# Kernel tuning notes

Hardware: AMD Instinct MI355X
Metric: run time of the kernel (lower is better)

Reference implementation:

```python
import jax, jax.numpy as jnp
import numpy as np

N_NODES = 50000
N_EDGES = 800000
IN_CH = 64
HID = 64
EDGE_DIM = 16


def _glorot(key, shape):
    fan_in, fan_out = shape[0], shape[1]
    lim = (6.0 / (fan_in + fan_out)) ** 0.5
    return jax.random.uniform(key, shape, jnp.float32, -lim, lim)


def setup_inputs() -> dict:
    key = jax.random.key(0)
    ks = jax.random.split(key, 12)
    x = jax.random.normal(ks[0], (N_NODES, IN_CH), jnp.float32)
    edge_index = jax.random.randint(ks[1], (2, N_EDGES), 0, N_NODES, jnp.int64)
    edge_attr = jax.random.normal(ks[2], (N_EDGES, EDGE_DIM), jnp.float32)
    # SAGEConv1: lin_l (aggregated neighbors, with bias) + lin_r (root, no bias)
    W1l = _glorot(ks[3], (IN_CH, HID)); b1l = jnp.zeros((HID,), jnp.float32)
    W1r = _glorot(ks[4], (IN_CH, HID))
    # SAGEConv2
    W2l = _glorot(ks[5], (HID, HID)); b2l = jnp.zeros((HID,), jnp.float32)
    W2r = _glorot(ks[6], (HID, HID))
    # edge MLP: Linear(2*HID+EDGE_DIM -> HID), ReLU, Linear(HID -> 1)
    Wm1 = _glorot(ks[7], (2 * HID + EDGE_DIM, HID))
    bm1 = jnp.zeros((HID,), jnp.float32)
    Wm2 = _glorot(ks[8], (HID, 1))
    bm2 = jnp.zeros((1,), jnp.float32)
    return dict(x=x, edge_index=edge_index, edge_attr=edge_attr,
                W1l=W1l, b1l=b1l, W1r=W1r,
                W2l=W2l, b2l=b2l, W2r=W2r,
                Wm1=Wm1, bm1=bm1, Wm2=Wm2, bm2=bm2)


def _sage_conv(x, src, dst, deg_inv, Wl, bl, Wr):
    # mean aggregation of source-node features at destination nodes
    n = x.shape[0]
    agg = jax.ops.segment_sum(x[src], dst, num_segments=n)  # [N, d]
    agg = agg * deg_inv  # mean over incoming edges
    return agg @ Wl + bl + x @ Wr


def reference(x, edge_index, edge_attr, W1l, b1l, W1r, W2l, b2l, W2r, Wm1, bm1, Wm2, bm2):
    src, dst = edge_index[0], edge_index[1]
    n = x.shape[0]
    # in-degree (over dst), clamped to 1 as in PyG mean aggregation
    deg = jax.ops.segment_sum(jnp.ones((src.shape[0],), x.dtype), dst, num_segments=n)
    deg_inv = (1.0 / jnp.maximum(deg, 1.0))[:, None]  # [N,1]

    h = jax.nn.relu(_sage_conv(x, src, dst, deg_inv, W1l, b1l, W1r))
    h = jax.nn.relu(_sage_conv(h, src, dst, deg_inv, W2l, b2l, W2r))

    # gather endpoint embeddings + concat with edge features -> MLP score
    edge_input = jnp.concatenate([h[src], h[dst], edge_attr], axis=-1)  # [E, 2H+De]
    hidden = jax.nn.relu(edge_input @ Wm1 + bm1)
    return (hidden @ Wm2 + bm2).squeeze(-1)  # [E]
```

## Files before the change

### kernel.cpp

```cpp
#include <hip/hip_runtime.h>
#include <hip/hip_bf16.h>


#define C 64
#define KP 168
#define SK 136
#define TILE_E 64
#define WSHIFT 12

typedef short short8 __attribute__((ext_vector_type(8)));
typedef float f32x4 __attribute__((ext_vector_type(4)));

__device__ __forceinline__ unsigned short f2bf(float f) {
    unsigned int u = __float_as_uint(f);
    return (unsigned short)((u + 0x7FFFu + ((u >> 16) & 1u)) >> 16);
}
__device__ __forceinline__ unsigned int pack2(float lo, float hi) {
    return (unsigned int)f2bf(lo) | ((unsigned int)f2bf(hi) << 16);
}
__device__ __forceinline__ float bflo(unsigned int u) { return __uint_as_float(u << 16); }
__device__ __forceinline__ float bfhi(unsigned int u) { return __uint_as_float(u & 0xFFFF0000u); }

__global__ void prep(const int* __restrict__ dst, int* __restrict__ degi,
                     const float* __restrict__ ea, unsigned short* __restrict__ eaB,
                     const float* __restrict__ x, unsigned short* __restrict__ xB,
                     int E, int nx8, int doEa) {
    int i = blockIdx.x * blockDim.x + threadIdx.x;
    if (i < E) atomicAdd(&degi[dst[i]], 1);
    if (doEa && i < 2 * E) {
        const float4* p = (const float4*)(ea + (size_t)i * 8);
        float4 a = p[0], b = p[1];
        uint4 o;
        o.x = pack2(a.x, a.y); o.y = pack2(a.z, a.w);
        o.z = pack2(b.x, b.y); o.w = pack2(b.z, b.w);
        *(uint4*)(eaB + (size_t)i * 8) = o;
    }
    if (i < nx8) {
        const float4* p = (const float4*)(x + (size_t)i * 8);
        float4 a = p[0], b = p[1];
        uint4 o;
        o.x = pack2(a.x, a.y); o.y = pack2(a.z, a.w);
        o.z = pack2(b.x, b.y); o.w = pack2(b.z, b.w);
        *(uint4*)(xB + (size_t)i * 8) = o;
    }
}

__global__ __launch_bounds__(256) void scan_partial(const int* __restrict__ degi,
        int* __restrict__ rowptr, int* __restrict__ partials, int N) {
    __shared__ int sWs[4];
    int t = threadIdx.x, b = blockIdx.x;
    int g0 = b * 1024 + t * 4;
    int v0 = (g0 + 0 < N) ? degi[g0 + 0] : 0;
    int v1 = (g0 + 1 < N) ? degi[g0 + 1] : 0;
    int v2 = (g0 + 2 < N) ? degi[g0 + 2] : 0;
    int v3 = (g0 + 3 < N) ? degi[g0 + 3] : 0;
    int tsum = v0 + v1 + v2 + v3;
    int lane = t & 63, w = t >> 6;
    int incl = tsum;
    #pragma unroll
    for (int m = 1; m < 64; m <<= 1) {
        int y = __shfl_up(incl, m, 64);
        if (lane >= m) incl += y;
    }
    if (lane == 63) sWs[w] = incl;
    __syncthreads();
    int wprefix = 0;
    for (int i = 0; i < w; ++i) wprefix += sWs[i];
    int run = wprefix + incl - tsum;
    if (g0 + 0 < N) rowptr[g0 + 0] = run; run += v0;
    if (g0 + 1 < N) rowptr[g0 + 1] = run; run += v1;
    if (g0 + 2 < N) rowptr[g0 + 2] = run; run += v2;
    if (g0 + 3 < N) rowptr[g0 + 3] = run;
    if (t == 255) partials[b] = wprefix + incl;
}

__global__ __launch_bounds__(256) void scan_add_fused(int* __restrict__ rowptr,
        const int* __restrict__ partials, int* __restrict__ cursor,
        const int* __restrict__ degi, float* __restrict__ deg_inv,
        int N, int E, int nb) {
    __shared__ int sOff[64];
    int t = threadIdx.x;
    if (t < 64) {
        int v = (t < nb) ? partials[t] : 0;
        int incl = v;
        #pragma unroll
        for (int m = 1; m < 64; m <<= 1) {
            int y = __shfl_up(incl, m, 64);
            if (t >= m) incl += y;
        }
        sOff[t] = incl - v;
    }
    __syncthreads();
    int i = blockIdx.x * 256 + t;
    if (i < N) {
        int r = rowptr[i] + sOff[i >> 10];
        rowptr[i] = r;
        cursor[i] = r;
        deg_inv[i] = 1.0f / fmaxf((float)degi[i], 1.0f);
    }
    if (i == 0) rowptr[N] = E;
}

__global__ __launch_bounds__(256) void fill_csr_xcd(const int* __restrict__ src,
        const int* __restrict__ dst, int* __restrict__ cursor,
        int* __restrict__ eSrc, int E) {
    int g = blockIdx.x & 7;
    int tid = (blockIdx.x >> 3) * 256 + threadIdx.x;
    int stride = (gridDim.x >> 3) * 256;
    for (int e = tid; e < E; e += stride) {
        int d = dst[e];
        if (((d >> WSHIFT) & 7) == g) {
            int pos = atomicAdd(&cursor[d], 1);
            eSrc[pos] = src[e];
        }
    }
}

__global__ __launch_bounds__(256) void csr_agg_np(const unsigned short* __restrict__ fB,
        const int* __restrict__ rowptr, const int* __restrict__ eSrc,
        const float* __restrict__ deg_inv, unsigned short* __restrict__ aggB, int N) {
    int wv = threadIdx.x >> 6;
    int lane = threadIdx.x & 63;
    int nl = lane & 7, cg = lane >> 3;
    int node = blockIdx.x * 32 + wv * 8 + nl;
    if (node >= N) return;
    int row = rowptr[node], end = rowptr[node + 1];
    float a[8] = {0.f, 0.f, 0.f, 0.f, 0.f, 0.f, 0.f, 0.f};
    int j = row;
    for (; j + 2 <= end; j += 2) {
        int s0 = eSrc[j];
        int s1 = eSrc[j + 1];
        uint4 v0 = *(const uint4*)(fB + (size_t)s0 * C + cg * 8);
        uint4 v1 = *(const uint4*)(fB + (size_t)s1 * C + cg * 8);
        a[0] += bflo(v0.x); a[1] += bfhi(v0.x);
        a[2] += bflo(v0.y); a[3] += bfhi(v0.y);
        a[4] += bflo(v0.z); a[5] += bfhi(v0.z);
        a[6] += bflo(v0.w); a[7] += bfhi(v0.w);
        a[0] += bflo(v1.x); a[1] += bfhi(v1.x);
        a[2] += bflo(v1.y); a[3] += bfhi(v1.y);
        a[4] += bflo(v1.z); a[5] += bfhi(v1.z);
        a[6] += bflo(v1.w); a[7] += bfhi(v1.w);
    }
    if (j < end) {
        int s = eSrc[j];
        uint4 v = *(const uint4*)(fB + (size_t)s * C + cg * 8);
        a[0] += bflo(v.x); a[1] += bfhi(v.x);
        a[2] += bflo(v.y); a[3] += bfhi(v.y);
        a[4] += bflo(v.z); a[5] += bfhi(v.z);
        a[6] += bflo(v.w); a[7] += bfhi(v.w);
    }
    float di = deg_inv[node];
    uint4 o;
    o.x = pack2(a[0] * di, a[1] * di);
    o.y = pack2(a[2] * di, a[3] * di);
    o.z = pack2(a[4] * di, a[5] * di);
    o.w = pack2(a[6] * di, a[7] * di);
    *(uint4*)(aggB + (size_t)node * C + cg * 8) = o;
}

__global__ __launch_bounds__(256) void dense_mfma(
        const unsigned short* __restrict__ aB, const unsigned short* __restrict__ xB,
        const float* __restrict__ Wl, const float* __restrict__ Wr,
        const float* __restrict__ bl, unsigned short* __restrict__ hOut, int N) {
    __shared__ unsigned short sW[C * SK];
    __shared__ unsigned short sAB[C * SK];
    int t = threadIdx.x;
    int lane = t & 63, w = t >> 6;
    int l15 = lane & 15, quad = lane >> 4;
    int n0 = blockIdx.x * 64;

    for (int i = t; i < 128 * C; i += 256) {
        int k = i >> 6, n = i & 63;
        float v = (k < C) ? Wl[k * C + n] : Wr[(k - C) * C + n];
        sW[n * SK + k] = f2bf(v);
    }
    for (int i = t; i < 64 * 16; i += 256) {
        int r = i >> 4, ch = i & 15;
        int node = n0 + r;
        uint4 v = {0u, 0u, 0u, 0u};
        if (node < N)
            v = (ch < 8) ? *(const uint4*)(aB + (size_t)node * C + ch * 8)
                         : *(const uint4*)(xB + (size_t)node * C + (ch - 8) * 8);
        *(uint4*)&sAB[r * SK + ch * 8] = v;
    }
    __syncthreads();

    short8 bW[4][4];
    #pragma unroll
    for (int t4 = 0; t4 < 4; ++t4)
        #pragma unroll
        for (int kc = 0; kc < 4; ++kc)
            bW[t4][kc] = *(const short8*)&sW[(t4 * 16 + l15) * SK + kc * 32 + quad * 8];
    float blr[4];
    #pragma unroll
    for (int t4 = 0; t4 < 4; ++t4) blr[t4] = bl[t4 * 16 + l15];

    f32x4 acc[4] = {{0.f, 0.f, 0.f, 0.f}, {0.f, 0.f, 0.f, 0.f},
                    {0.f, 0.f, 0.f, 0.f}, {0.f, 0.f, 0.f, 0.f}};
    #pragma unroll
    for (int kc = 0; kc < 4; ++kc) {
        short8 a = *(const short8*)&sAB[(w * 16 + l15) * SK + kc * 32 + quad * 8];
        #pragma unroll
        for (int t4 = 0; t4 < 4; ++t4)
            acc[t4] = __builtin_amdgcn_mfma_f32_16x16x32_bf16(a, bW[t4][kc], acc[t4], 0, 0, 0);
    }
    __syncthreads();

    #pragma unroll
    for (int t4 = 0; t4 < 4; ++t4)
        #pragma unroll
        for (int r = 0; r < 4; ++r) {
            int rl = w * 16 + quad * 4 + r;
            sW[rl * 72 + t4 * 16 + l15] = f2bf(fmaxf(acc[t4][r] + blr[t4], 0.f));
        }
    __syncthreads();
    for (int i = t; i < 64 * 8; i += 256) {
        int r = i >> 3, c8 = i & 7;
        int node = n0 + r;
        if (node < N)
            *(uint4*)(hOut + (size_t)node * C + c8 * 8) = *(const uint4*)&sW[r * 72 + c8 * 8];
    }
}

template <bool EAB>
__device__ __forceinline__ void gather_rows(const unsigned short* __restrict__ hB,
        const unsigned short* __restrict__ eaB, const float* __restrict__ ea,
        int s, int d, int idxc, int quad,
        uint4& u0, uint4& u1, uint4& u2, uint4& u3, uint4& u4) {
    const uint4* ps = (const uint4*)(hB + (size_t)s * C);
    const uint4* pd = (const uint4*)(hB + (size_t)d * C);
    u0 = ps[quad];
    u1 = ps[4 + quad];
    u2 = pd[quad];
    u3 = pd[4 + quad];
    u4.x = 0u; u4.y = 0u; u4.z = 0u; u4.w = 0u;
    if (quad < 2) {
        if (EAB) {
            u4 = *(const uint4*)(eaB + (size_t)idxc * 16 + quad * 8);
        } else {
            const float4* pe = (const float4*)(ea + (size_t)idxc * 16 + quad * 8);
            float4 f0 = pe[0], f1 = pe[1];
            u4.x = pack2(f0.x, f0.y); u4.y = pack2(f0.z, f0.w);
            u4.z = pack2(f1.x, f1.y); u4.w = pack2(f1.z, f1.w);
        }
    }
}

template <bool EAB>
__global__ __launch_bounds__(256) void edge_mlp_pipe(
        const unsigned short* __restrict__ hB, const int* __restrict__ src,
        const int* __restrict__ dst, const float* __restrict__ ea,
        const unsigned short* __restrict__ eaB,
        const float* __restrict__ Wm1, const float* __restrict__ bm1,
        const float* __restrict__ Wm2, const float* __restrict__ bm2,
        float* __restrict__ out, int E, int nTiles) {
    __shared__ unsigned short sW[C * KP];
    int t = threadIdx.x;
    int lane = t & 63, w = t >> 6;
    int l15 = lane & 15, quad = lane >> 4;

    for (int i = t; i < C * 3; i += 256) {
        int r = i / 3, cc = 144 + (i % 3) * 8;
        uint4 z = {0u, 0u, 0u, 0u};
        *(uint4*)&sW[r * KP + cc] = z;
    }
    for (int i = t; i < 144 * C; i += 256) {
        int k = i >> 6, n = i & 63;
        sW[n * KP + k] = f2bf(Wm1[i]);
    }
    __syncthreads();

    short8 bW[4][5];
    #pragma unroll
    for (int t4 = 0; t4 < 4; ++t4)
        #pragma unroll
        for (int kc = 0; kc < 5; ++kc)
            bW[t4][kc] = *(const short8*)&sW[(t4 * 16 + l15) * KP + kc * 32 + quad * 8];
    float bmr[4], w2r[4];
    #pragma unroll
    for (int t4 = 0; t4 < 4; ++t4) {
        int j = t4 * 16 + l15;
        bmr[t4] = bm1[j];
        w2r[t4] = Wm2[j];
    }
    float bb = bm2[0];

    int stride = gridDim.x;
    int lbase = w * 16 + l15;

    int tile = blockIdx.x;
    int idxc = min(tile * TILE_E + lbase, E - 1);
    int s = src[idxc], d = dst[idxc];
    int tileN = tile + stride;
    int idxNc = (tileN < nTiles) ? min(tileN * TILE_E + lbase, E - 1) : idxc;
    int sN = src[idxNc], dN = dst[idxNc];
    uint4 cu0, cu1, cu2, cu3, cu4;
    gather_rows<EAB>(hB, eaB, ea, s, d, idxc, quad, cu0, cu1, cu2, cu3, cu4);

    while (true) {
        bool hasNext = (tileN < nTiles);
        uint4 nu0, nu1, nu2, nu3, nu4;
        gather_rows<EAB>(hB, eaB, ea, sN, dN, idxNc, quad, nu0, nu1, nu2, nu3, nu4);
        int tileNN = tileN + stride;
        int idxNNc = (tileNN < nTiles) ? min(tileNN * TILE_E + lbase, E - 1) : idxNc;
        int sNN = src[idxNNc], dNN = dst[idxNNc];

        short8 a0 = *(short8*)&cu0, a1 = *(short8*)&cu1, a2 = *(short8*)&cu2,
               a3 = *(short8*)&cu3, a4 = *(short8*)&cu4;
        f32x4 acc[4] = {{0.f, 0.f, 0.f, 0.f}, {0.f, 0.f, 0.f, 0.f},
                        {0.f, 0.f, 0.f, 0.f}, {0.f, 0.f, 0.f, 0.f}};
        #pragma unroll
        for (int t4 = 0; t4 < 4; ++t4) {
            acc[t4] = __builtin_amdgcn_mfma_f32_16x16x32_bf16(a0, bW[t4][0], acc[t4], 0, 0, 0);
            acc[t4] = __builtin_amdgcn_mfma_f32_16x16x32_bf16(a1, bW[t4][1], acc[t4], 0, 0, 0);
            acc[t4] = __builtin_amdgcn_mfma_f32_16x16x32_bf16(a2, bW[t4][2], acc[t4], 0, 0, 0);
            acc[t4] = __builtin_amdgcn_mfma_f32_16x16x32_bf16(a3, bW[t4][3], acc[t4], 0, 0, 0);
            acc[t4] = __builtin_amdgcn_mfma_f32_16x16x32_bf16(a4, bW[t4][4], acc[t4], 0, 0, 0);
        }

        float sres[4];
        #pragma unroll
        for (int r = 0; r < 4; ++r) {
            float v = 0.f;
            #pragma unroll
            for (int t4 = 0; t4 < 4; ++t4)
                v += fmaxf(acc[t4][r] + bmr[t4], 0.f) * w2r[t4];
            #pragma unroll
            for (int m = 1; m < 16; m <<= 1)
                v += __shfl_xor(v, m, 16);
            sres[r] = v;
        }
        if (l15 == 0) {
            int e0 = tile * TILE_E;
            #pragma unroll
            for (int r = 0; r < 4; ++r) {
                int e = e0 + w * 16 + quad * 4 + r;
                if (e < E) out[e] = sres[r] + bb;
            }
        }

        if (!hasNext) break;
        tile = tileN; tileN = tileNN;
        idxc = idxNc; idxNc = idxNNc;
        s = sN; sN = sNN; d = dN; dN = dNN;
        cu0 = nu0; cu1 = nu1; cu2 = nu2; cu3 = nu3; cu4 = nu4;
    }
}

extern "C" void kernel_launch(void* const* d_in, const int* in_sizes, int n_in,
                              void* d_out, int out_size, void* d_ws, size_t ws_size,
                              hipStream_t stream) {
    const float* x   = (const float*)d_in[0];
    const int*   ei  = (const int*)d_in[1];
    const float* ea  = (const float*)d_in[2];
    const float* W1l = (const float*)d_in[3];
    const float* b1l = (const float*)d_in[4];
    const float* W1r = (const float*)d_in[5];
    const float* W2l = (const float*)d_in[6];
    const float* b2l = (const float*)d_in[7];
    const float* W2r = (const float*)d_in[8];
    const float* Wm1 = (const float*)d_in[9];
    const float* bm1 = (const float*)d_in[10];
    const float* Wm2 = (const float*)d_in[11];
    const float* bm2 = (const float*)d_in[12];
    float* out = (float*)d_out;

    const int N = in_sizes[0] / C;
    const int E = in_sizes[1] / 2;
    const int* src = ei;
    const int* dst = ei + E;

    char* wsb = (char*)d_ws;
    int npad = (N + 1023) & ~1023;
    float* deg_inv = (float*)wsb;                wsb += (size_t)npad * 4;
    unsigned short* xB   = (unsigned short*)wsb; wsb += (size_t)npad * C * 2;
    unsigned short* h1B  = (unsigned short*)wsb; wsb += (size_t)npad * C * 2;
    unsigned short* h2B  = (unsigned short*)wsb; wsb += (size_t)npad * C * 2;
    unsigned short* aggB = (unsigned short*)wsb; wsb += (size_t)npad * C * 2;
    int* degi    = (int*)wsb;                    wsb += (size_t)npad * 4;
    int* rowptr  = (int*)wsb;                    wsb += (size_t)(npad + 64) * 4;
    int* cursor  = (int*)wsb;                    wsb += (size_t)npad * 4;
    int* eSrc    = (int*)wsb;                    wsb += (size_t)E * 4;
    int* partials = (int*)wsb;                   wsb += 64 * 4;
    unsigned short* eaB = (unsigned short*)wsb;
    size_t used = (size_t)(wsb - (char*)d_ws);
    int useEaB = (ws_size >= used + (size_t)E * 16 * 2) ? 1 : 0;

    int tpb = 256;
    int nb = (N + 1023) / 1024;
    int nx8 = N * C / 8;

    hipMemsetAsync(degi, 0, (size_t)N * sizeof(int), stream);
    int prepN = (2 * E > nx8) ? 2 * E : nx8;
    prep<<<(prepN + tpb - 1) / tpb, tpb, 0, stream>>>(dst, degi, ea, eaB, x, xB, E, nx8, useEaB);
    scan_partial<<<nb, tpb, 0, stream>>>(degi, rowptr, partials, N);
    scan_add_fused<<<(N + tpb - 1) / tpb, tpb, 0, stream>>>(rowptr, partials, cursor,
            degi, deg_inv, N, E, nb);
    fill_csr_xcd<<<2048, tpb, 0, stream>>>(src, dst, cursor, eSrc, E);

    int aggGrid = (N + 31) / 32;
    csr_agg_np<<<aggGrid, tpb, 0, stream>>>(xB, rowptr, eSrc, deg_inv, aggB, N);
    dense_mfma<<<(N + 63) / 64, tpb, 0, stream>>>(aggB, xB, W1l, W1r, b1l, h1B, N);

    csr_agg_np<<<aggGrid, tpb, 0, stream>>>(h1B, rowptr, eSrc, deg_inv, aggB, N);
    dense_mfma<<<(N + 63) / 64, tpb, 0, stream>>>(aggB, h1B, W2l, W2r, b2l, h2B, N);

    int nTiles = (E + TILE_E - 1) / TILE_E;
    int grid = nTiles < 2048 ? nTiles : 2048;
    if (useEaB)
        edge_mlp_pipe<true><<<grid, tpb, 0, stream>>>(h2B, src, dst, ea, eaB,
                Wm1, bm1, Wm2, bm2, out, E, nTiles);
    else
        edge_mlp_pipe<false><<<grid, tpb, 0, stream>>>(h2B, src, dst, ea, eaB,
                Wm1, bm1, Wm2, bm2, out, E, nTiles);
}
```

Measured before the change: 300.0 us.

## Process edge MLP in CSR-sorted order with permuted edge attributes

While building the CSR, the fill kernel now also writes each edge's destination, original index and a bf16 copy of its attributes into dst-sorted position. A new edge MLP kernel walks edges in this sorted order, so the dst-row gathers hit the same node repeatedly and reuse cache, then scatters results back through the stored index. This costs extra writes in the CSR fill, 40 bytes more workspace per edge, and scattered output stores.

```diff
diff --git a/kernel.cpp b/kernel.cpp
--- a/kernel.cpp
+++ b/kernel.cpp
@@ -112,6 +112,33 @@
         if (((d >> WSHIFT) & 7) == g) {
             int pos = atomicAdd(&cursor[d], 1);
             eSrc[pos] = src[e];
+        }
+    }
+}
+
+__global__ __launch_bounds__(256) void fill_csr_perm(const int* __restrict__ src,
+        const int* __restrict__ dst, const float* __restrict__ ea,
+        int* __restrict__ cursor, int* __restrict__ eSrc, int* __restrict__ eDst,
+        int* __restrict__ eIdx, unsigned short* __restrict__ eaP, int E) {
+    int g = blockIdx.x & 7;
+    int tid = (blockIdx.x >> 3) * 256 + threadIdx.x;
+    int stride = (gridDim.x >> 3) * 256;
+    for (int e = tid; e < E; e += stride) {
+        int d = dst[e];
+        if (((d >> WSHIFT) & 7) == g) {
+            int pos = atomicAdd(&cursor[d], 1);
+            eSrc[pos] = src[e];
+            eDst[pos] = d;
+            eIdx[pos] = e;
+            const float4* p = (const float4*)(ea + (size_t)e * 16);
+            float4 a = p[0], b = p[1], c = p[2], f = p[3];
+            uint4 o0, o1;
+            o0.x = pack2(a.x, a.y); o0.y = pack2(a.z, a.w);
+            o0.z = pack2(b.x, b.y); o0.w = pack2(b.z, b.w);
+            o1.x = pack2(c.x, c.y); o1.y = pack2(c.z, c.w);
+            o1.z = pack2(f.x, f.y); o1.w = pack2(f.z, f.w);
+            uint4* q = (uint4*)(eaP + (size_t)pos * 16);
+            q[0] = o0; q[1] = o1;
         }
     }
 }
@@ -246,6 +273,106 @@
     }
 }
 
+__global__ __launch_bounds__(256) void edge_mlp_perm(
+        const unsigned short* __restrict__ hB, const int* __restrict__ eSrc,
+        const int* __restrict__ eDst, const int* __restrict__ eIdx,
+        const unsigned short* __restrict__ eaP,
+        const float* __restrict__ Wm1, const float* __restrict__ bm1,
+        const float* __restrict__ Wm2, const float* __restrict__ bm2,
+        float* __restrict__ out, int E, int nTiles) {
+    __shared__ unsigned short sW[C * KP];
+    int t = threadIdx.x;
+    int lane = t & 63, w = t >> 6;
+    int l15 = lane & 15, quad = lane >> 4;
+
+    for (int i = t; i < C * 3; i += 256) {
+        int r = i / 3, cc = 144 + (i % 3) * 8;
+        uint4 z = {0u, 0u, 0u, 0u};
+        *(uint4*)&sW[r * KP + cc] = z;
+    }
+    for (int i = t; i < 144 * C; i += 256) {
+        int k = i >> 6, n = i & 63;
+        sW[n * KP + k] = f2bf(Wm1[i]);
+    }
+    __syncthreads();
+
+    short8 bW[4][5];
+    #pragma unroll
+    for (int t4 = 0; t4 < 4; ++t4)
+        #pragma unroll
+        for (int kc = 0; kc < 5; ++kc)
+            bW[t4][kc] = *(const short8*)&sW[(t4 * 16 + l15) * KP + kc * 32 + quad * 8];
+    float bmr[4], w2r[4];
+    #pragma unroll
+    for (int t4 = 0; t4 < 4; ++t4) {
+        int j = t4 * 16 + l15;
+        bmr[t4] = bm1[j];
+        w2r[t4] = Wm2[j];
+    }
+    float bb = bm2[0];
+
+    int stride = gridDim.x;
+    int lbase = w * 16 + l15;
+
+    int tile = blockIdx.x;
+    int p = min(tile * TILE_E + lbase, E - 1);
+    int s = eSrc[p], d = eDst[p];
+    int tileN = tile + stride;
+    int pN = (tileN < nTiles) ? min(tileN * TILE_E + lbase, E - 1) : p;
+    int sN = eSrc[pN], dN = eDst[pN];
+    uint4 cu0, cu1, cu2, cu3, cu4;
+    gather_rows<true>(hB, eaP, (const float*)0, s, d, p, quad, cu0, cu1, cu2, cu3, cu4);
+
+    while (true) {
+        bool hasNext = (tileN < nTiles);
+        uint4 nu0, nu1, nu2, nu3, nu4;
+        gather_rows<true>(hB, eaP, (const float*)0, sN, dN, pN, quad, nu0, nu1, nu2, nu3, nu4);
+        int tileNN = tileN + stride;
+        int pNN = (tileNN < nTiles) ? min(tileNN * TILE_E + lbase, E - 1) : pN;
+        int sNN = eSrc[pNN], dNN = eDst[pNN];
+
+        short8 a0 = *(short8*)&cu0, a1 = *(short8*)&cu1, a2 = *(short8*)&cu2,
+               a3 = *(short8*)&cu3, a4 = *(short8*)&cu4;
+        f32x4 acc[4] = {{0.f, 0.f, 0.f, 0.f}, {0.f, 0.f, 0.f, 0.f},
+                        {0.f, 0.f, 0.f, 0.f}, {0.f, 0.f, 0.f, 0.f}};
+        #pragma unroll
+        for (int t4 = 0; t4 < 4; ++t4) {
+            acc[t4] = __builtin_amdgcn_mfma_f32_16x16x32_bf16(a0, bW[t4][0], acc[t4], 0, 0, 0);
+            acc[t4] = __builtin_amdgcn_mfma_f32_16x16x32_bf16(a1, bW[t4][1], acc[t4], 0, 0, 0);
+            acc[t4] = __builtin_amdgcn_mfma_f32_16x16x32_bf16(a2, bW[t4][2], acc[t4], 0, 0, 0);
+            acc[t4] = __builtin_amdgcn_mfma_f32_16x16x32_bf16(a3, bW[t4][3], acc[t4], 0, 0, 0);
+            acc[t4] = __builtin_amdgcn_mfma_f32_16x16x32_bf16(a4, bW[t4][4], acc[t4], 0, 0, 0);
+        }
+
+        float sres[4];
+        #pragma unroll
+        for (int r = 0; r < 4; ++r) {
+            float v = 0.f;
+            #pragma unroll
+            for (int t4 = 0; t4 < 4; ++t4)
+                v += fmaxf(acc[t4][r] + bmr[t4], 0.f) * w2r[t4];
+            #pragma unroll
+            for (int m = 1; m < 16; m <<= 1)
+                v += __shfl_xor(v, m, 16);
+            sres[r] = v;
+        }
+        if (l15 == 0) {
+            int e0 = tile * TILE_E;
+            #pragma unroll
+            for (int r = 0; r < 4; ++r) {
+                int pp = e0 + w * 16 + quad * 4 + r;
+                if (pp < E) out[eIdx[pp]] = sres[r] + bb;
+            }
+        }
+
+        if (!hasNext) break;
+        tile = tileN; tileN = tileNN;
+        p = pN; pN = pNN;
+        s = sN; sN = sNN; d = dN; dN = dNN;
+        cu0 = nu0; cu1 = nu1; cu2 = nu2; cu3 = nu3; cu4 = nu4;
+    }
+}
+
 template <bool EAB>
 __global__ __launch_bounds__(256) void edge_mlp_pipe(
         const unsigned short* __restrict__ hB, const int* __restrict__ src,
@@ -382,21 +509,30 @@
     int* cursor  = (int*)wsb;                    wsb += (size_t)npad * 4;
     int* eSrc    = (int*)wsb;                    wsb += (size_t)E * 4;
     int* partials = (int*)wsb;                   wsb += 64 * 4;
+    size_t used = (size_t)(wsb - (char*)d_ws);
+    int* eIdx = (int*)wsb;
+    int* eDst = (int*)(wsb + (size_t)E * 4);
+    unsigned short* eaP = (unsigned short*)(wsb + (size_t)E * 8);
+    int usePerm = (ws_size >= used + (size_t)E * 8 + (size_t)E * 32) ? 1 : 0;
     unsigned short* eaB = (unsigned short*)wsb;
-    size_t used = (size_t)(wsb - (char*)d_ws);
-    int useEaB = (ws_size >= used + (size_t)E * 16 * 2) ? 1 : 0;
+    int useEaB = (ws_size >= used + (size_t)E * 32) ? 1 : 0;
 
     int tpb = 256;
     int nb = (N + 1023) / 1024;
     int nx8 = N * C / 8;
 
     hipMemsetAsync(degi, 0, (size_t)N * sizeof(int), stream);
-    int prepN = (2 * E > nx8) ? 2 * E : nx8;
-    prep<<<(prepN + tpb - 1) / tpb, tpb, 0, stream>>>(dst, degi, ea, eaB, x, xB, E, nx8, useEaB);
+    int prepN = ((usePerm ? E : 2 * E) > nx8) ? (usePerm ? E : 2 * E) : nx8;
+    prep<<<(prepN + tpb - 1) / tpb, tpb, 0, stream>>>(dst, degi, ea, eaB, x, xB,
+            E, nx8, usePerm ? 0 : useEaB);
     scan_partial<<<nb, tpb, 0, stream>>>(degi, rowptr, partials, N);
     scan_add_fused<<<(N + tpb - 1) / tpb, tpb, 0, stream>>>(rowptr, partials, cursor,
             degi, deg_inv, N, E, nb);
-    fill_csr_xcd<<<2048, tpb, 0, stream>>>(src, dst, cursor, eSrc, E);
+    if (usePerm)
+        fill_csr_perm<<<2048, tpb, 0, stream>>>(src, dst, ea, cursor, eSrc, eDst,
+                eIdx, eaP, E);
+    else
+        fill_csr_xcd<<<2048, tpb, 0, stream>>>(src, dst, cursor, eSrc, E);
 
     int aggGrid = (N + 31) / 32;
     csr_agg_np<<<aggGrid, tpb, 0, stream>>>(xB, rowptr, eSrc, deg_inv, aggB, N);
@@ -407,7 +543,10 @@
 
     int nTiles = (E + TILE_E - 1) / TILE_E;
     int grid = nTiles < 2048 ? nTiles : 2048;
-    if (useEaB)
+    if (usePerm)
+        edge_mlp_perm<<<grid, tpb, 0, stream>>>(h2B, eSrc, eDst, eIdx, eaP,
+                Wm1, bm1, Wm2, bm2, out, E, nTiles);
+    else if (useEaB)
         edge_mlp_pipe<true><<<grid, tpb, 0, stream>>>(h2B, src, dst, ea, eaB,
                 Wm1, bm1, Wm2, bm2, out, E, nTiles);
     else
```

After: 371.2 us. +23.7%, slower.
